# Optimization experiments

Measured on AMD Instinct MI355X. Metric: run time of the kernel, lower is better.

## Reference

```python
import jax, jax.numpy as jnp
import numpy as np

N = 100_000      # nodes
E = 2_500_000    # edges (nnz), avg degree 25
D_IN = 32
D_OUT = 32


def setup_inputs() -> dict:
    key = jax.random.key(0)
    k1, k2, k3, k4 = jax.random.split(key, 4)
    X = jax.random.normal(k1, (N, D_IN), dtype=jnp.float32)
    # CSR row offsets: sorted, anchored at 0 and E
    rp = jnp.sort(jax.random.randint(k2, (N + 1,), 0, E, dtype=jnp.int32))
    rp = rp.at[0].set(0).at[-1].set(E)
    ci = jax.random.randint(k3, (E,), 0, N, dtype=jnp.int32)
    W = (jax.random.normal(k4, (D_IN, D_OUT), dtype=jnp.float32)
         * (1.0 / np.sqrt(D_OUT)).astype(np.float32))
    dummy = jnp.zeros((1,), dtype=jnp.int32)
    return {
        "X": X,
        "weights": W,
        "row_pointers": rp,
        "column_index": ci,
        "blockPartition": dummy,
        "edgeToColumn": dummy,
        "edgeToRow": dummy,
        "hybrid_type": dummy,
        "row_nzr": dummy,
        "col_nzr": dummy,
    }


def reference(X, weights, row_pointers, column_index, blockPartition,
              edgeToColumn, edgeToRow, hybrid_type, row_nzr, col_nzr):
    # Fused GIN: X_prime = A @ X (CSR neighbor sum), then X_prime @ W.
    # Recover per-edge destination row from CSR offsets: row r owns edges
    # in [row_pointers[r], row_pointers[r+1]).
    edge_ids = jnp.arange(E, dtype=row_pointers.dtype)
    row = jnp.searchsorted(row_pointers, edge_ids, side="right") - 1  # [E]
    gathered = X[column_index]                       # [E, D_IN] (irregular gather)
    X_prime = jax.ops.segment_sum(gathered, row, num_segments=N)  # [N, D_IN]
    return X_prime @ weights                          # [N, D_OUT]
```

## Files before the change

### kernel.cpp

```cpp
#include <hip/hip_runtime.h>

#define D 32

__global__ __launch_bounds__(256, 4)
void gin_fused(const float* __restrict__ X,
               const float* __restrict__ W,
               const int* __restrict__ rp,
               const int* __restrict__ ci,
               float* __restrict__ out,
               int n) {
    __shared__ float Wl[D * D];

    int tid = threadIdx.x;
    {
        const float4* Wv = (const float4*)W;
        float4* Wlv = (float4*)Wl;
        Wlv[tid] = Wv[tid];
    }
    __syncthreads();

    int wave = tid >> 6;
    int lane = tid & 63;
    int row = blockIdx.x * 4 + wave;
    if (row >= n) return;

    int start = rp[row];
    int deg   = rp[row + 1] - start;

    int g = lane >> 3;
    int s = lane & 7;

    float4 acc = make_float4(0.f, 0.f, 0.f, 0.f);

    for (int cb = 0; cb < deg; cb += 64) {
        int rem = deg - cb;
        int nv  = rem < 64 ? rem : 64;
        int myci = (lane < nv) ? ci[start + cb + lane] : 0;

        {
            float4 x[4]; float m[4];
            #pragma unroll
            for (int it = 0; it < 4; ++it) {
                int l = it * 8 + g;
                int c = __shfl(myci, l, 64);
                m[it] = (l < rem) ? 1.f : 0.f;
                x[it] = ((const float4*)(X + (size_t)c * D))[s];
            }
            #pragma unroll
            for (int it = 0; it < 4; ++it) {
                acc.x = fmaf(m[it], x[it].x, acc.x);
                acc.y = fmaf(m[it], x[it].y, acc.y);
                acc.z = fmaf(m[it], x[it].z, acc.z);
                acc.w = fmaf(m[it], x[it].w, acc.w);
            }
        }
        if (rem > 32) {
            float4 x[4]; float m[4];
            #pragma unroll
            for (int it = 0; it < 4; ++it) {
                int l = (it + 4) * 8 + g;
                int c = __shfl(myci, l, 64);
                m[it] = (l < rem) ? 1.f : 0.f;
                x[it] = ((const float4*)(X + (size_t)c * D))[s];
            }
            #pragma unroll
            for (int it = 0; it < 4; ++it) {
                acc.x = fmaf(m[it], x[it].x, acc.x);
                acc.y = fmaf(m[it], x[it].y, acc.y);
                acc.z = fmaf(m[it], x[it].z, acc.z);
                acc.w = fmaf(m[it], x[it].w, acc.w);
            }
        }
    }

    #pragma unroll
    for (int off = 8; off < 64; off <<= 1) {
        acc.x += __shfl_xor(acc.x, off, 64);
        acc.y += __shfl_xor(acc.y, off, 64);
        acc.z += __shfl_xor(acc.z, off, 64);
        acc.w += __shfl_xor(acc.w, off, 64);
    }

    int j = lane & 31;
    float o = 0.f;
    #pragma unroll
    for (int sg = 0; sg < 8; ++sg) {
        float ax = __shfl(acc.x, sg, 64);
        float ay = __shfl(acc.y, sg, 64);
        float az = __shfl(acc.z, sg, 64);
        float aw = __shfl(acc.w, sg, 64);
        int d = 4 * sg;
        o = fmaf(ax, Wl[(d    ) * D + j], o);
        o = fmaf(ay, Wl[(d + 1) * D + j], o);
        o = fmaf(az, Wl[(d + 2) * D + j], o);
        o = fmaf(aw, Wl[(d + 3) * D + j], o);
    }
    if (lane < 32) out[(size_t)row * D + j] = o;
}

extern "C" void kernel_launch(void* const* d_in, const int* in_sizes, int n_in,
                              void* d_out, int out_size, void* d_ws, size_t ws_size,
                              hipStream_t stream) {
    const float* X  = (const float*)d_in[0];
    const float* W  = (const float*)d_in[1];
    const int*   rp = (const int*)d_in[2];
    const int*   ci = (const int*)d_in[3];
    float* out = (float*)d_out;

    int n = in_sizes[2] - 1;
    int blocks = (n + 3) / 4;
    hipLaunchKernelGGL(gin_fused, dim3(blocks), dim3(256), 0, stream,
                       X, W, rp, ci, out, n);
}
```

Before: 152.5 us.

## Precompute X@W then aggregate transformed rows with degree-specialized gathers

Uses associativity (A·X)·W = A·(X·W) to first compute Y = X·W in a separate kernel into workspace, with an extra zero row at index n. The aggregation kernel then gathers rows of Y instead of X, and padding lanes point at the zero row so the per-edge mask multiplies are dropped. A switch on the number of valid 8-edge groups unrolls only as many loads as needed per chunk. This trades an extra pass over X and a write/read of Y, plus a second launch, for removing masked loads and the per-row matvec epilogue. It falls back to the fused kernel when the workspace is too small.

```diff
diff --git a/kernel.cpp b/kernel.cpp
--- a/kernel.cpp
+++ b/kernel.cpp
@@ -1,6 +1,100 @@
 #include <hip/hip_runtime.h>
 
 #define D 32
+
+__global__ __launch_bounds__(256, 8)
+void xw_kernel(const float* __restrict__ X, const float* __restrict__ W,
+               float* __restrict__ Y, int n) {
+    const int lane = threadIdx.x & 63;
+    const int j    = lane & 31;
+    const int wid  = blockIdx.x * (blockDim.x >> 6) + (threadIdx.x >> 6);
+    const int nw   = gridDim.x * (blockDim.x >> 6);
+
+    float w[D];
+    #pragma unroll
+    for (int d = 0; d < D; ++d) w[d] = W[d * D + j];
+
+    for (int r = wid; r <= n; r += nw) {
+        float o0 = 0.f, o1 = 0.f;
+        if (r < n) {
+            const float* xr =
+                X + (size_t)(unsigned)__builtin_amdgcn_readfirstlane(r) * D;
+            #pragma unroll
+            for (int d = 0; d < D; d += 2) {
+                o0 = fmaf(xr[d],     w[d],     o0);
+                o1 = fmaf(xr[d + 1], w[d + 1], o1);
+            }
+        }
+        if (lane < 32) Y[(size_t)r * D + j] = o0 + o1;
+    }
+}
+
+template <int K>
+__device__ __forceinline__ void gather_acc(const float* __restrict__ Y,
+                                           int myci, int base, int g, int s,
+                                           float4& acc) {
+    float4 x[K];
+    #pragma unroll
+    for (int it = 0; it < K; ++it) {
+        int c = __shfl(myci, (base + it) * 8 + g, 64);
+        x[it] = ((const float4*)(Y + (size_t)(unsigned)c * D))[s];
+    }
+    #pragma unroll
+    for (int it = 0; it < K; ++it) {
+        acc.x += x[it].x; acc.y += x[it].y;
+        acc.z += x[it].z; acc.w += x[it].w;
+    }
+}
+
+__global__ __launch_bounds__(256, 8)
+void agg_kernel(const float* __restrict__ Y, const int* __restrict__ rp,
+                const int* __restrict__ ci, float* __restrict__ out, int n) {
+    const int tid  = threadIdx.x;
+    const int wave = tid >> 6;
+    const int lane = tid & 63;
+    int row = blockIdx.x * 4 + wave;
+    if (row >= n) return;
+    row = __builtin_amdgcn_readfirstlane(row);
+
+    const int start = rp[row];
+    const int deg   = rp[row + 1] - start;
+
+    const int g  = lane >> 3;
+    const int s  = lane & 7;
+    const int zr = n;
+
+    float4 acc = make_float4(0.f, 0.f, 0.f, 0.f);
+
+    for (int cb = 0; cb < deg; cb += 64) {
+        const int rem  = deg - cb;
+        const int nv   = rem < 64 ? rem : 64;
+        const int myci = (lane < nv) ? ci[start + cb + lane] : zr;
+
+        switch ((nv + 7) >> 3) {
+            case 1: gather_acc<1>(Y, myci, 0, g, s, acc); break;
+            case 2: gather_acc<2>(Y, myci, 0, g, s, acc); break;
+            case 3: gather_acc<3>(Y, myci, 0, g, s, acc); break;
+            case 4: gather_acc<4>(Y, myci, 0, g, s, acc); break;
+            case 5: gather_acc<4>(Y, myci, 0, g, s, acc);
+                    gather_acc<1>(Y, myci, 4, g, s, acc); break;
+            case 6: gather_acc<4>(Y, myci, 0, g, s, acc);
+                    gather_acc<2>(Y, myci, 4, g, s, acc); break;
+            case 7: gather_acc<4>(Y, myci, 0, g, s, acc);
+                    gather_acc<3>(Y, myci, 4, g, s, acc); break;
+            default: gather_acc<4>(Y, myci, 0, g, s, acc);
+                     gather_acc<4>(Y, myci, 4, g, s, acc); break;
+        }
+    }
+
+    #pragma unroll
+    for (int off = 8; off < 64; off <<= 1) {
+        acc.x += __shfl_xor(acc.x, off, 64);
+        acc.y += __shfl_xor(acc.y, off, 64);
+        acc.z += __shfl_xor(acc.z, off, 64);
+        acc.w += __shfl_xor(acc.w, off, 64);
+    }
+    if (lane < 8) ((float4*)(out + (size_t)row * D))[s] = acc;
+}
 
 __global__ __launch_bounds__(256, 4)
 void gin_fused(const float* __restrict__ X,
@@ -36,7 +130,6 @@
         int rem = deg - cb;
         int nv  = rem < 64 ? rem : 64;
         int myci = (lane < nv) ? ci[start + cb + lane] : 0;
-
         {
             float4 x[4]; float m[4];
             #pragma unroll
@@ -108,7 +201,16 @@
     float* out = (float*)d_out;
 
     int n = in_sizes[2] - 1;
-    int blocks = (n + 3) / 4;
-    hipLaunchKernelGGL(gin_fused, dim3(blocks), dim3(256), 0, stream,
-                       X, W, rp, ci, out, n);
-}
+    size_t ybytes = (size_t)(n + 1) * D * sizeof(float);
+
+    if (ws_size >= ybytes) {
+        float* Y = (float*)d_ws;
+        hipLaunchKernelGGL(xw_kernel, dim3(1024), dim3(256), 0, stream,
+                           X, W, Y, n);
+        hipLaunchKernelGGL(agg_kernel, dim3((n + 3) / 4), dim3(256), 0, stream,
+                           Y, rp, ci, out, n);
+    } else {
+        hipLaunchKernelGGL(gin_fused, dim3((n + 3) / 4), dim3(256), 0, stream,
+                           X, W, rp, ci, out, n);
+    }
+}
```

Result: faster. 132.8 us (-12.9%).

## Reorder GIN as A@(X@W) with separate transform and row-per-group aggregation kernels

Applied to the files above, without the earlier changes.

Computes Y = X@W first into workspace, then aggregates neighbor rows of Y per node, using the associativity of the matmul. The aggregation kernel assigns one row per 8-lane group, so each wave handles 8 rows with 4 independent loads in flight. This drops the per-row shuffle reduction and in-kernel matmul and avoids masked lanes for short rows. It adds an extra launch and a write/read of an N×32 intermediate, and may diverge within a wave when row degrees vary. It falls back to the fused kernel if workspace is too small.

```diff
diff --git a/kernel.cpp b/kernel.cpp
--- a/kernel.cpp
+++ b/kernel.cpp
@@ -1,6 +1,75 @@
 #include <hip/hip_runtime.h>
 
 #define D 32
+
+__global__ __launch_bounds__(256, 8)
+void xw_kernel(const float* __restrict__ X, const float* __restrict__ W,
+               float* __restrict__ Y, int n) {
+    const int lane = threadIdx.x & 63;
+    const int j    = lane & 31;
+    const int h    = lane >> 5;
+    const int wid  = (blockIdx.x * blockDim.x + threadIdx.x) >> 6;
+    const int nw   = (gridDim.x * blockDim.x) >> 6;
+
+    float w[D];
+    #pragma unroll
+    for (int d = 0; d < D; ++d) w[d] = W[d * D + j];
+
+    for (int r0 = 2 * wid; r0 <= n; r0 += 2 * nw) {
+        const int r = r0 + h;
+        float o = 0.f;
+        if (r < n) {
+            const float4* xr = (const float4*)(X + (size_t)r * D);
+            #pragma unroll
+            for (int k = 0; k < 8; ++k) {
+                float4 xv = xr[k];
+                o = fmaf(xv.x, w[4 * k    ], o);
+                o = fmaf(xv.y, w[4 * k + 1], o);
+                o = fmaf(xv.z, w[4 * k + 2], o);
+                o = fmaf(xv.w, w[4 * k + 3], o);
+            }
+        }
+        if (r <= n) Y[(size_t)r * D + j] = o;
+    }
+}
+
+__global__ __launch_bounds__(256, 8)
+void agg_kernel(const float* __restrict__ Y, const int* __restrict__ rp,
+                const int* __restrict__ ci, float* __restrict__ out, int n) {
+    const int lane = threadIdx.x & 63;
+    const int g    = lane >> 3;
+    const int s    = lane & 7;
+    const int wid  = (blockIdx.x * blockDim.x + threadIdx.x) >> 6;
+
+    const int r = wid * 8 + g;
+    if (r >= n) return;
+
+    const int start = rp[r];
+    const int deg   = rp[r + 1] - start;
+    const int* cp   = ci + start;
+
+    float4 acc = make_float4(0.f, 0.f, 0.f, 0.f);
+
+    int t = 0;
+    for (; t + 4 <= deg; t += 4) {
+        int c0 = cp[t], c1 = cp[t + 1], c2 = cp[t + 2], c3 = cp[t + 3];
+        float4 x0 = ((const float4*)(Y + (size_t)(unsigned)c0 * D))[s];
+        float4 x1 = ((const float4*)(Y + (size_t)(unsigned)c1 * D))[s];
+        float4 x2 = ((const float4*)(Y + (size_t)(unsigned)c2 * D))[s];
+        float4 x3 = ((const float4*)(Y + (size_t)(unsigned)c3 * D))[s];
+        acc.x += (x0.x + x1.x) + (x2.x + x3.x);
+        acc.y += (x0.y + x1.y) + (x2.y + x3.y);
+        acc.z += (x0.z + x1.z) + (x2.z + x3.z);
+        acc.w += (x0.w + x1.w) + (x2.w + x3.w);
+    }
+    for (; t < deg; ++t) {
+        int c = cp[t];
+        float4 x = ((const float4*)(Y + (size_t)(unsigned)c * D))[s];
+        acc.x += x.x; acc.y += x.y; acc.z += x.z; acc.w += x.w;
+    }
+
+    ((float4*)(out + (size_t)r * D))[s] = acc;
+}
 
 __global__ __launch_bounds__(256, 4)
 void gin_fused(const float* __restrict__ X,
@@ -36,7 +105,6 @@
         int rem = deg - cb;
         int nv  = rem < 64 ? rem : 64;
         int myci = (lane < nv) ? ci[start + cb + lane] : 0;
-
         {
             float4 x[4]; float m[4];
             #pragma unroll
@@ -108,7 +176,17 @@
     float* out = (float*)d_out;
 
     int n = in_sizes[2] - 1;
-    int blocks = (n + 3) / 4;
-    hipLaunchKernelGGL(gin_fused, dim3(blocks), dim3(256), 0, stream,
-                       X, W, rp, ci, out, n);
+    size_t ybytes = (size_t)(n + 1) * D * sizeof(float);
+
+    if (ws_size >= ybytes) {
+        float* Y = (float*)d_ws;
+        hipLaunchKernelGGL(xw_kernel, dim3(2048), dim3(256), 0, stream,
+                           X, W, Y, n);
+        int blocks = (n + 31) / 32;
+        hipLaunchKernelGGL(agg_kernel, dim3(blocks), dim3(256), 0, stream,
+                           Y, rp, ci, out, n);
+    } else {
+        hipLaunchKernelGGL(gin_fused, dim3((n + 3) / 4), dim3(256), 0, stream,
+                           X, W, rp, ci, out, n);
+    }
 }
```

New measurement: 165.9 us. 8.8% more time.
